# Kernel optimization log

Measured on AMD Instinct MI355X. Metric: run time of the kernel, lower is better.

Reference implementation:

```python
import jax, jax.numpy as jnp
import numpy as np

PADDED_NODE_ID = -1


def setup_inputs() -> dict:
    key = jax.random.key(0)
    k0, k1, k2, k3 = jax.random.split(key, 4)
    B, N, F = 1024, 512, 64
    src_ids = jax.random.randint(k0, (B, N), 0, 1000, dtype=jnp.int64 if jax.config.jax_enable_x64 else jnp.int32)
    dst_ids = jax.random.randint(k1, (B, N), 0, 1000, dtype=src_ids.dtype)
    W1 = jax.random.normal(k2, (1, F), dtype=jnp.float32) * 0.1   # Linear(1 -> F)
    b1 = jnp.zeros((F,), dtype=jnp.float32)
    W2 = jax.random.normal(k3, (F, F), dtype=jnp.float32) * 0.05  # Linear(F -> F)
    b2 = jnp.zeros((F,), dtype=jnp.float32)
    return {"src_ids": src_ids, "dst_ids": dst_ids, "W1": W1, "b1": b1, "W2": W2, "b2": b2}


def _count_freqs(src_ids, dst_ids):
    # For each row, count occurrences of each neighbor id within its own row
    # and within the paired row (cross-lookup). Equivalent to np.unique counts
    # plus dict-based cross mapping in the original, vectorized as pairwise
    # equality reductions over [B, N, N].
    def eq_count(a, b):
        return (a[:, :, None] == b[:, None, :]).sum(-1).astype(jnp.float32)  # [B, N]

    src_in_src = eq_count(src_ids, src_ids)
    src_in_dst = eq_count(src_ids, dst_ids)
    dst_in_dst = eq_count(dst_ids, dst_ids)
    dst_in_src = eq_count(dst_ids, src_ids)

    source_freq = jnp.stack([src_in_src, src_in_dst], axis=-1)  # [B, N, 2]
    dst_freq = jnp.stack([dst_in_dst, dst_in_src], axis=-1)     # [B, N, 2]

    # zero out padded positions
    source_freq = jnp.where((src_ids == PADDED_NODE_ID)[..., None], 0.0, source_freq)
    dst_freq = jnp.where((dst_ids == PADDED_NODE_ID)[..., None], 0.0, dst_freq)
    return source_freq, dst_freq


def reference(src_ids, dst_ids, W1, b1, W2, b2):
    source_freq, dst_freq = _count_freqs(src_ids, dst_ids)  # [B, N, 2] each

    def encode(freq):
        # freq[..., None] has shape [B, N, 2, 1]; Linear(1->F) is an outer product
        h = jax.nn.relu(freq[..., None] * W1[0] + b1)        # [B, N, 2, F]
        h = jnp.einsum('bnkf,fg->bnkg', h, W2) + b2          # [B, N, 2, F]
        return h.sum(axis=2)                                 # [B, N, F]

    return encode(source_freq), encode(dst_freq)
```

## Files before the change

kernel.cpp:

```cpp
#include <hip/hip_runtime.h>

#define BATCH 1024
#define NSEQ  512
#define NF    64
#define TBL_N (NSEQ + 1)
#define HIST_BINS 1024

typedef float f32x4 __attribute__((ext_vector_type(4)));

__global__ void build_table_kernel(const float* __restrict__ W1,
                                   const float* __restrict__ b1,
                                   const float* __restrict__ W2,
                                   const float* __restrict__ b2,
                                   float* __restrict__ tbl) {
    const int c = blockIdx.x;
    const int g = threadIdx.x;
    const float cf = (float)c;
    float acc = b2[g];
#pragma unroll 8
    for (int f = 0; f < NF; ++f) {
        float h = fmaxf(cf * W1[f] + b1[f], 0.0f);
        acc += h * W2[f * NF + g];
    }
    tbl[c * NF + g] = acc;
}

__global__ __launch_bounds__(256) void count_kernel(
        const int* __restrict__ src_ids,
        const int* __restrict__ dst_ids,
        ushort4* __restrict__ counts) {
    __shared__ int s_src[NSEQ];
    __shared__ int s_dst[NSEQ];
    __shared__ int hist_s[HIST_BINS];
    __shared__ int hist_d[HIST_BINS];

    const int b = blockIdx.x;
    const int t = threadIdx.x;

#pragma unroll
    for (int i = t; i < HIST_BINS; i += 256) { hist_s[i] = 0; hist_d[i] = 0; }
#pragma unroll
    for (int i = t; i < NSEQ; i += 256) {
        s_src[i] = src_ids[(size_t)b * NSEQ + i];
        s_dst[i] = dst_ids[(size_t)b * NSEQ + i];
    }
    __syncthreads();

#pragma unroll
    for (int i = t; i < NSEQ; i += 256) {
        int si = s_src[i], di = s_dst[i];
        if (si >= 0) atomicAdd(&hist_s[si], 1);
        if (di >= 0) atomicAdd(&hist_d[di], 1);
    }
    __syncthreads();

#pragma unroll
    for (int i = t; i < NSEQ; i += 256) {
        int si = s_src[i], di = s_dst[i];
        ushort4 p;
        p.x = (si >= 0) ? (unsigned short)hist_s[si] : 0;
        p.y = (si >= 0) ? (unsigned short)hist_d[si] : 0;
        p.z = (di >= 0) ? (unsigned short)hist_d[di] : 0;
        p.w = (di >= 0) ? (unsigned short)hist_s[di] : 0;
        counts[(size_t)b * NSEQ + i] = p;
    }
}

__global__ __launch_bounds__(256) void expand_kernel(
        const ushort4* __restrict__ counts,
        const float* __restrict__ tbl,
        float* __restrict__ out_src,
        float* __restrict__ out_dst) {
    const f32x4* __restrict__ tbl4 = (const f32x4*)tbl;
    f32x4* __restrict__ o0 = (f32x4*)out_src;
    f32x4* __restrict__ o1 = (f32x4*)out_dst;
    const long total  = (long)BATCH * NSEQ * (NF / 4);
    const long stride = (long)gridDim.x * blockDim.x;
    for (long e = (long)blockIdx.x * blockDim.x + threadIdx.x; e < total; e += stride) {
        const long n  = e >> 4;
        const int  f4 = (int)(e & 15);
        const ushort4 c = counts[n];
        f32x4 a0 = tbl4[(int)c.x * (NF / 4) + f4];
        f32x4 a1 = tbl4[(int)c.y * (NF / 4) + f4];
        __builtin_nontemporal_store(a0 + a1, &o0[e]);
        f32x4 d0 = tbl4[(int)c.z * (NF / 4) + f4];
        f32x4 d1 = tbl4[(int)c.w * (NF / 4) + f4];
        __builtin_nontemporal_store(d0 + d1, &o1[e]);
    }
}

__global__ __launch_bounds__(256) void cooc_encode_kernel(
        const int* __restrict__ src_ids,
        const int* __restrict__ dst_ids,
        const float* __restrict__ tbl,
        float* __restrict__ out_src,
        float* __restrict__ out_dst) {
    __shared__ int s_src[NSEQ];
    __shared__ int s_dst[NSEQ];
    __shared__ int hist_s[HIST_BINS];
    __shared__ int hist_d[HIST_BINS];
    __shared__ int c_ss[NSEQ], c_sd[NSEQ], c_dd[NSEQ], c_ds[NSEQ];

    const int b = blockIdx.x;
    const int t = threadIdx.x;

#pragma unroll
    for (int i = t; i < HIST_BINS; i += 256) { hist_s[i] = 0; hist_d[i] = 0; }
#pragma unroll
    for (int i = t; i < NSEQ; i += 256) {
        s_src[i] = src_ids[(size_t)b * NSEQ + i];
        s_dst[i] = dst_ids[(size_t)b * NSEQ + i];
    }
    __syncthreads();
#pragma unroll
    for (int i = t; i < NSEQ; i += 256) {
        int si = s_src[i], di = s_dst[i];
        if (si >= 0) atomicAdd(&hist_s[si], 1);
        if (di >= 0) atomicAdd(&hist_d[di], 1);
    }
    __syncthreads();
#pragma unroll
    for (int i = t; i < NSEQ; i += 256) {
        int si = s_src[i], di = s_dst[i];
        c_ss[i] = (si >= 0) ? hist_s[si] : 0;
        c_sd[i] = (si >= 0) ? hist_d[si] : 0;
        c_dd[i] = (di >= 0) ? hist_d[di] : 0;
        c_ds[i] = (di >= 0) ? hist_s[di] : 0;
    }
    __syncthreads();

    const float4* __restrict__ tbl4 = (const float4*)tbl;
    float4* __restrict__ o0 = (float4*)(out_src + (size_t)b * NSEQ * NF);
    float4* __restrict__ o1 = (float4*)(out_dst + (size_t)b * NSEQ * NF);
    const int NV = NSEQ * NF / 4;
#pragma unroll 4
    for (int e = t; e < NV; e += 256) {
        int n  = e >> 4;
        int f4 = e & 15;
        float4 a0 = tbl4[c_ss[n] * (NF / 4) + f4];
        float4 a1 = tbl4[c_sd[n] * (NF / 4) + f4];
        o0[e] = make_float4(a0.x + a1.x, a0.y + a1.y, a0.z + a1.z, a0.w + a1.w);
        float4 d0 = tbl4[c_dd[n] * (NF / 4) + f4];
        float4 d1 = tbl4[c_ds[n] * (NF / 4) + f4];
        o1[e] = make_float4(d0.x + d1.x, d0.y + d1.y, d0.z + d1.z, d0.w + d1.w);
    }
}

extern "C" void kernel_launch(void* const* d_in, const int* in_sizes, int n_in,
                              void* d_out, int out_size, void* d_ws, size_t ws_size,
                              hipStream_t stream) {
    const int*   src_ids = (const int*)d_in[0];
    const int*   dst_ids = (const int*)d_in[1];
    const float* W1 = (const float*)d_in[2];
    const float* b1 = (const float*)d_in[3];
    const float* W2 = (const float*)d_in[4];
    const float* b2 = (const float*)d_in[5];

    float* out_src = (float*)d_out;
    float* out_dst = (float*)d_out + (size_t)BATCH * NSEQ * NF;

    const size_t tbl_bytes    = (size_t)TBL_N * NF * sizeof(float);
    const size_t counts_off   = (tbl_bytes + 255) & ~(size_t)255;
    const size_t counts_bytes = (size_t)BATCH * NSEQ * sizeof(ushort4);

    float* tbl = (float*)d_ws;

    build_table_kernel<<<TBL_N, NF, 0, stream>>>(W1, b1, W2, b2, tbl);

    if (ws_size >= counts_off + counts_bytes) {
        ushort4* counts = (ushort4*)((char*)d_ws + counts_off);
        count_kernel<<<BATCH, 256, 0, stream>>>(src_ids, dst_ids, counts);
        expand_kernel<<<2048, 256, 0, stream>>>(counts, tbl, out_src, out_dst);
    } else {
        cooc_encode_kernel<<<BATCH, 256, 0, stream>>>(src_ids, dst_ids, tbl,
                                                      out_src, out_dst);
    }
}
```

Measured before the change: 63.04 us.

## Merge table build into count kernel and restructure expand per row/output

Fuses the table-building work into the count kernel as extra blocks, removing one kernel launch. The expand kernel now assigns one block per (row, output) pair, stages that row's two counts in shared memory, and writes a single output. It also switches from nontemporal to regular stores. The aim is to cut launch overhead and redundant count loads, at the cost of losing the nontemporal store hint.

```diff
diff --git a/kernel.cpp b/kernel.cpp
--- a/kernel.cpp
+++ b/kernel.cpp
@@ -6,7 +6,105 @@
 #define TBL_N (NSEQ + 1)
 #define HIST_BINS 1024
 
-typedef float f32x4 __attribute__((ext_vector_type(4)));
+#define TBL_BLOCKS ((TBL_N + 3) / 4)
+
+__global__ __launch_bounds__(256) void prep_kernel(
+        const int* __restrict__ src_ids,
+        const int* __restrict__ dst_ids,
+        const float* __restrict__ W1,
+        const float* __restrict__ b1,
+        const float* __restrict__ W2,
+        const float* __restrict__ b2,
+        float* __restrict__ tbl,
+        ushort4* __restrict__ counts) {
+    const int t = threadIdx.x;
+
+    if (blockIdx.x >= BATCH) {
+        const int c = (blockIdx.x - BATCH) * 4 + (t >> 6);
+        const int g = t & 63;
+        if (c < TBL_N) {
+            const float cf = (float)c;
+            float acc = b2[g];
+#pragma unroll 8
+            for (int f = 0; f < NF; ++f) {
+                float h = fmaxf(cf * W1[f] + b1[f], 0.0f);
+                acc += h * W2[f * NF + g];
+            }
+            tbl[c * NF + g] = acc;
+        }
+        return;
+    }
+
+    __shared__ int s_src[NSEQ];
+    __shared__ int s_dst[NSEQ];
+    __shared__ int hist_s[HIST_BINS];
+    __shared__ int hist_d[HIST_BINS];
+
+    const int b = blockIdx.x;
+
+#pragma unroll
+    for (int i = t; i < HIST_BINS; i += 256) { hist_s[i] = 0; hist_d[i] = 0; }
+#pragma unroll
+    for (int i = t; i < NSEQ; i += 256) {
+        s_src[i] = src_ids[(size_t)b * NSEQ + i];
+        s_dst[i] = dst_ids[(size_t)b * NSEQ + i];
+    }
+    __syncthreads();
+
+#pragma unroll
+    for (int i = t; i < NSEQ; i += 256) {
+        int si = s_src[i], di = s_dst[i];
+        if (si >= 0) atomicAdd(&hist_s[si], 1);
+        if (di >= 0) atomicAdd(&hist_d[di], 1);
+    }
+    __syncthreads();
+
+#pragma unroll
+    for (int i = t; i < NSEQ; i += 256) {
+        int si = s_src[i], di = s_dst[i];
+        ushort4 p;
+        p.x = (si >= 0) ? (unsigned short)hist_s[si] : 0;
+        p.y = (si >= 0) ? (unsigned short)hist_d[si] : 0;
+        p.z = (di >= 0) ? (unsigned short)hist_d[di] : 0;
+        p.w = (di >= 0) ? (unsigned short)hist_s[di] : 0;
+        counts[(size_t)b * NSEQ + i] = p;
+    }
+}
+
+__global__ __launch_bounds__(256) void expand_kernel(
+        const ushort4* __restrict__ counts,
+        const float* __restrict__ tbl,
+        float* __restrict__ out_src,
+        float* __restrict__ out_dst) {
+    __shared__ ushort2 s_cnt[NSEQ];
+
+    const int t = threadIdx.x;
+    const int which = blockIdx.x >> 10;
+    const int row   = blockIdx.x & 1023;
+
+    const ushort4* __restrict__ crow = counts + (size_t)row * NSEQ;
+#pragma unroll
+    for (int i = t; i < NSEQ; i += 256) {
+        ushort4 c = crow[i];
+        s_cnt[i] = (which == 0) ? make_ushort2(c.x, c.y) : make_ushort2(c.z, c.w);
+    }
+    __syncthreads();
+
+    const float4* __restrict__ tbl4 = (const float4*)tbl;
+    float* base = (which == 0) ? out_src : out_dst;
+    float4* __restrict__ o = (float4*)(base + (size_t)row * NSEQ * NF);
+
+    const int NV = NSEQ * NF / 4;
+#pragma unroll 8
+    for (int e = t; e < NV; e += 256) {
+        int n  = e >> 4;
+        int f4 = e & 15;
+        ushort2 c = s_cnt[n];
+        float4 a0 = tbl4[(int)c.x * (NF / 4) + f4];
+        float4 a1 = tbl4[(int)c.y * (NF / 4) + f4];
+        o[e] = make_float4(a0.x + a1.x, a0.y + a1.y, a0.z + a1.z, a0.w + a1.w);
+    }
+}
 
 __global__ void build_table_kernel(const float* __restrict__ W1,
                                    const float* __restrict__ b1,
@@ -23,70 +121,6 @@
         acc += h * W2[f * NF + g];
     }
     tbl[c * NF + g] = acc;
-}
-
-__global__ __launch_bounds__(256) void count_kernel(
-        const int* __restrict__ src_ids,
-        const int* __restrict__ dst_ids,
-        ushort4* __restrict__ counts) {
-    __shared__ int s_src[NSEQ];
-    __shared__ int s_dst[NSEQ];
-    __shared__ int hist_s[HIST_BINS];
-    __shared__ int hist_d[HIST_BINS];
-
-    const int b = blockIdx.x;
-    const int t = threadIdx.x;
-
-#pragma unroll
-    for (int i = t; i < HIST_BINS; i += 256) { hist_s[i] = 0; hist_d[i] = 0; }
-#pragma unroll
-    for (int i = t; i < NSEQ; i += 256) {
-        s_src[i] = src_ids[(size_t)b * NSEQ + i];
-        s_dst[i] = dst_ids[(size_t)b * NSEQ + i];
-    }
-    __syncthreads();
-
-#pragma unroll
-    for (int i = t; i < NSEQ; i += 256) {
-        int si = s_src[i], di = s_dst[i];
-        if (si >= 0) atomicAdd(&hist_s[si], 1);
-        if (di >= 0) atomicAdd(&hist_d[di], 1);
-    }
-    __syncthreads();
-
-#pragma unroll
-    for (int i = t; i < NSEQ; i += 256) {
-        int si = s_src[i], di = s_dst[i];
-        ushort4 p;
-        p.x = (si >= 0) ? (unsigned short)hist_s[si] : 0;
-        p.y = (si >= 0) ? (unsigned short)hist_d[si] : 0;
-        p.z = (di >= 0) ? (unsigned short)hist_d[di] : 0;
-        p.w = (di >= 0) ? (unsigned short)hist_s[di] : 0;
-        counts[(size_t)b * NSEQ + i] = p;
-    }
-}
-
-__global__ __launch_bounds__(256) void expand_kernel(
-        const ushort4* __restrict__ counts,
-        const float* __restrict__ tbl,
-        float* __restrict__ out_src,
-        float* __restrict__ out_dst) {
-    const f32x4* __restrict__ tbl4 = (const f32x4*)tbl;
-    f32x4* __restrict__ o0 = (f32x4*)out_src;
-    f32x4* __restrict__ o1 = (f32x4*)out_dst;
-    const long total  = (long)BATCH * NSEQ * (NF / 4);
-    const long stride = (long)gridDim.x * blockDim.x;
-    for (long e = (long)blockIdx.x * blockDim.x + threadIdx.x; e < total; e += stride) {
-        const long n  = e >> 4;
-        const int  f4 = (int)(e & 15);
-        const ushort4 c = counts[n];
-        f32x4 a0 = tbl4[(int)c.x * (NF / 4) + f4];
-        f32x4 a1 = tbl4[(int)c.y * (NF / 4) + f4];
-        __builtin_nontemporal_store(a0 + a1, &o0[e]);
-        f32x4 d0 = tbl4[(int)c.z * (NF / 4) + f4];
-        f32x4 d1 = tbl4[(int)c.w * (NF / 4) + f4];
-        __builtin_nontemporal_store(d0 + d1, &o1[e]);
-    }
 }
 
 __global__ __launch_bounds__(256) void cooc_encode_kernel(
@@ -165,13 +199,13 @@
 
     float* tbl = (float*)d_ws;
 
-    build_table_kernel<<<TBL_N, NF, 0, stream>>>(W1, b1, W2, b2, tbl);
-
     if (ws_size >= counts_off + counts_bytes) {
         ushort4* counts = (ushort4*)((char*)d_ws + counts_off);
-        count_kernel<<<BATCH, 256, 0, stream>>>(src_ids, dst_ids, counts);
-        expand_kernel<<<2048, 256, 0, stream>>>(counts, tbl, out_src, out_dst);
+        prep_kernel<<<BATCH + TBL_BLOCKS, 256, 0, stream>>>(
+            src_ids, dst_ids, W1, b1, W2, b2, tbl, counts);
+        expand_kernel<<<2 * BATCH, 256, 0, stream>>>(counts, tbl, out_src, out_dst);
     } else {
+        build_table_kernel<<<TBL_N, NF, 0, stream>>>(W1, b1, W2, b2, tbl);
         cooc_encode_kernel<<<BATCH, 256, 0, stream>>>(src_ids, dst_ids, tbl,
                                                       out_src, out_dst);
     }
```

Result: faster. 51.41 us (-18.5%).
